# Performance work log

Hardware: AMD Instinct MI355X
Metric: run time of the kernel (lower is better)

The kernel has to match this reference:

```python
import jax, jax.numpy as jnp
import numpy as np

H, IN, L, R = 128, 64, 3, 7
Nc, Na, Nx = 10000, 40000, 100000
NS = (Nc, Na, Nx)
ES = (50000, 100000, 100000, 150000, 200000, 200000, 200000)
# relation order: cc, c->a, a->c, aa, a->x, x->a, xx  (0=core,1=agg,2=access)
SRC_T = (0, 0, 1, 1, 1, 2, 2)
DST_T = (0, 1, 0, 1, 2, 1, 2)


def setup_inputs() -> dict:
    key = jax.random.key(0)
    ks = iter(jax.random.split(key, 80))
    d = {}
    for name, n in (("x_core", Nc), ("x_agg", Na), ("x_access", Nx)):
        d[name] = jax.random.normal(next(ks), (n, IN), jnp.float32)
    for r in range(R):
        d[f"src{r}"] = jax.random.randint(next(ks), (ES[r],), 0, NS[SRC_T[r]])
        d[f"dst{r}"] = jax.random.randint(next(ks), (ES[r],), 0, NS[DST_T[r]])
        d[f"ea{r}"] = jax.random.normal(next(ks), (ES[r], 3), jnp.float32)

    def w(k, shape, fan):
        return (jax.random.normal(k, shape, jnp.float32) / np.float32(np.sqrt(fan)))

    for nt in ("core", "agg", "access"):
        d[f"linW_{nt}"] = w(next(ks), (IN, H), IN)
        d[f"linb_{nt}"] = jnp.zeros((H,), jnp.float32)
    d["eW"] = w(next(ks), (L, R, 3, H), 3)       # GINEConv edge Linear(3->H)
    d["eb"] = jnp.zeros((L, R, H), jnp.float32)
    d["W1"] = w(next(ks), (L, R, H, H), H)        # MLP first Linear
    d["b1"] = jnp.zeros((L, R, H), jnp.float32)
    d["g1"] = jnp.ones((L, R, H), jnp.float32)    # BatchNorm gamma
    d["be1"] = jnp.zeros((L, R, H), jnp.float32)  # BatchNorm beta
    d["W2"] = w(next(ks), (L, R, H, H), H)        # MLP second Linear
    d["b2"] = jnp.zeros((L, R, H), jnp.float32)
    return d


def _forward(x_core, x_agg, x_access,
             linW_core, linb_core, linW_agg, linb_agg, linW_access, linb_access,
             eW, eb, W1, b1, g1, be1, W2, b2, srcs, dsts, eas):
    elu = jax.nn.elu
    h = [elu(x_core @ linW_core + linb_core),
         elu(x_agg @ linW_agg + linb_agg),
         elu(x_access @ linW_access + linb_access)]
    bn_inv = 1.0 / jnp.sqrt(jnp.float32(1.0 + 1e-5))  # eval BN: running mean 0, var 1
    for l in range(L):
        out = [jnp.zeros_like(ht) for ht in h]
        for r in range(R):
            s, t = SRC_T[r], DST_T[r]
            # GINEConv message: ReLU(x_j + Lin(edge_attr))  -> [E, H]
            msg = jax.nn.relu(h[s][srcs[r]] + eas[r] @ eW[l, r] + eb[l, r])
            agg = jax.ops.segment_sum(msg, dsts[r], num_segments=h[t].shape[0])
            z = h[t] + agg  # (1+eps)*x_i + aggr, eps=0
            # PyG MLP([H,H,H]): Linear -> BatchNorm -> ReLU -> Linear
            z = jax.nn.relu((z @ W1[l, r] + b1[l, r]) * bn_inv * g1[l, r] + be1[l, r])
            out[t] = out[t] + (z @ W2[l, r] + b2[l, r])  # HeteroConv aggr='sum'
        # residual + ELU; dropout is identity in eval mode
        h = [elu(out[t] + h[t]) for t in range(3)]
    return tuple(h)


def reference(x_core, x_agg, x_access,
              src0, dst0, ea0, src1, dst1, ea1, src2, dst2, ea2,
              src3, dst3, ea3, src4, dst4, ea4, src5, dst5, ea5,
              src6, dst6, ea6,
              linW_core, linb_core, linW_agg, linb_agg, linW_access, linb_access,
              eW, eb, W1, b1, g1, be1, W2, b2):
    srcs = (src0, src1, src2, src3, src4, src5, src6)
    dsts = (dst0, dst1, dst2, dst3, dst4, dst5, dst6)
    eas = (ea0, ea1, ea2, ea3, ea4, ea5, ea6)
    return _forward(x_core, x_agg, x_access,
                    linW_core, linb_core, linW_agg, linb_agg, linW_access, linb_access,
                    eW, eb, W1, b1, g1, be1, W2, b2, srcs, dsts, eas)
```

## Files before the change

### kernel.cpp

```cpp
#include <hip/hip_runtime.h>
#include <math.h>

#define H 128

typedef __attribute__((ext_vector_type(8))) short short8;
typedef __attribute__((ext_vector_type(4))) float f32x4;

static const int SRC_T_[7] = {0, 0, 1, 1, 1, 2, 2};
static const int DST_T_[7] = {0, 1, 0, 1, 2, 1, 2};

__device__ __forceinline__ float eluf(float x) {
    return x > 0.f ? x : (__expf(x) - 1.f);
}
__device__ __forceinline__ unsigned short f2bf(float x) {
    union { float f; unsigned int u; } v; v.f = x;
    unsigned int r = v.u + 0x7fffu + ((v.u >> 16) & 1u);
    return (unsigned short)(r >> 16);
}
__device__ __forceinline__ float bf2f(unsigned int u) {
    union { unsigned int u; float f; } v; v.u = u << 16;
    return v.f;
}

#define GLDS16(gp, lp) __builtin_amdgcn_global_load_lds( \
    (const __attribute__((address_space(1))) void*)(gp), \
    (__attribute__((address_space(3))) void*)(lp), 16, 0, 0)

struct PreCtx {
    const int* dst[7];
    int* deg;
    int E[7], bOff[8], hOff[8];
    const float* W1; const float* W2; const float* linW[3];
    unsigned short* wp; unsigned short* wlin;
    int gEnd;
};

__global__ __launch_bounds__(256) void k_pre(PreCtx P)
{
    const int b = blockIdx.x;
    const int tid = threadIdx.x;

    if (b < P.hOff[7]) {
        int r = 0;
        while (b >= P.hOff[r + 1]) ++r;
        const int lb = b - P.hOff[r];
        const int nb = P.hOff[r + 1] - P.hOff[r];
        const int* dst = P.dst[r];
        int* degr = P.deg + (P.bOff[r] << 8);
        for (int e = lb * 256 + tid; e < P.E[r]; e += nb * 256)
            atomicAdd(&degr[dst[e]], 1);
        return;
    }
    {
        const int lb = b - P.hOff[7];
        const int gw = P.gEnd - P.hOff[7];
        for (int i = lb * 256 + tid; i < 21 * 16384; i += gw * 256) {
            int lr = i >> 14, rem = i & 16383;
            int c = rem >> 7, k = rem & 127;
            P.wp[(size_t)(lr * 2 + 0) * 16384 + rem] = f2bf(P.W1[(size_t)lr * 16384 + k * H + c]);
            P.wp[(size_t)(lr * 2 + 1) * 16384 + rem] = f2bf(P.W2[(size_t)lr * 16384 + k * H + c]);
        }
        for (int i = lb * 256 + tid; i < 3 * 8192; i += gw * 256) {
            int t = i >> 13, rem = i & 8191;
            int c = rem >> 6, k = rem & 63;
            P.wlin[t * 8192 + c * 64 + k] = f2bf(P.linW[t][k * H + c]);
        }
    }
}

struct InCtx {
    const float* x[3]; const float* linb[3];
    unsigned short* hb[3]; int n[3];
    int gend[3];
};

__global__ __launch_bounds__(512, 2) void k_input_mfma(
    InCtx I, const unsigned short* __restrict__ wlin)
{
    __shared__ unsigned short xb[128 * 64];
    __shared__ unsigned short ob[128 * H];

    const int b = blockIdx.x;
    const int t = (b >= I.gend[0] ? 1 : 0) + (b >= I.gend[1] ? 1 : 0);
    const int lb = b - (t == 0 ? 0 : I.gend[t - 1]);
    const int n = I.n[t];
    const int tid = threadIdx.x;
    const int lane = tid & 63;
    const int wave = tid >> 6;
    const int wr = wave >> 2;
    const int wc = wave & 3;
    const int l15 = lane & 15;
    const int lq  = lane >> 4;
    const int c0 = wc * 32 + l15;
    const int r0 = lb * 128;
    const int rows = min(128, n - r0);
    const float* x = I.x[t];

    for (int idx = tid; idx < 128 * 16; idx += 512) {
        const int row = idx >> 4, cg = (idx & 15) << 2;
        uint2 p;
        if (row < rows) {
            f32x4 v = *(const f32x4*)&x[(size_t)(r0 + row) * 64 + cg];
            p.x = (unsigned int)f2bf(v.x) | ((unsigned int)f2bf(v.y) << 16);
            p.y = (unsigned int)f2bf(v.z) | ((unsigned int)f2bf(v.w) << 16);
        } else { p.x = 0; p.y = 0; }
        *(uint2*)&xb[row * 64 + (cg ^ ((row & 7) << 3))] = p;
    }
    const unsigned short* wt = wlin + (size_t)t * 8192;
    short8 wf[2][2];
#pragma unroll
    for (int nf = 0; nf < 2; ++nf)
#pragma unroll
        for (int kc = 0; kc < 2; ++kc)
            wf[nf][kc] = *(const short8*)&wt[(c0 + nf * 16) * 64 + kc * 32 + (lq << 3)];
    const float bc0 = I.linb[t][c0], bc1 = I.linb[t][c0 + 16];
    __syncthreads();

    const f32x4 Z4 = {0.f, 0.f, 0.f, 0.f};
    f32x4 acc[4][2];
#pragma unroll
    for (int rb = 0; rb < 4; ++rb)
#pragma unroll
        for (int nf = 0; nf < 2; ++nf) acc[rb][nf] = Z4;
#pragma unroll
    for (int kc = 0; kc < 2; ++kc) {
        const int kb = kc * 32 + (lq << 3);
        short8 af[4];
#pragma unroll
        for (int rb = 0; rb < 4; ++rb) {
            const int row = wr * 64 + rb * 16 + l15;
            af[rb] = *(const short8*)&xb[row * 64 + (kb ^ ((row & 7) << 3))];
        }
#pragma unroll
        for (int rb = 0; rb < 4; ++rb)
#pragma unroll
            for (int nf = 0; nf < 2; ++nf)
                acc[rb][nf] = __builtin_amdgcn_mfma_f32_16x16x32_bf16(
                    af[rb], wf[nf][kc], acc[rb][nf], 0, 0, 0);
    }
#pragma unroll
    for (int rb = 0; rb < 4; ++rb)
#pragma unroll
        for (int nf = 0; nf < 2; ++nf) {
            const int col = c0 + nf * 16;
            const float bc = nf == 0 ? bc0 : bc1;
#pragma unroll
            for (int rg = 0; rg < 4; ++rg) {
                const int row = wr * 64 + rb * 16 + (lq << 2) + rg;
                ob[row * H + col] = f2bf(eluf(acc[rb][nf][rg] + bc));
            }
        }
    __syncthreads();
    uint2* d = (uint2*)&I.hb[t][(size_t)r0 * H];
    const uint2* s2 = (const uint2*)ob;
    for (int idx = tid; idx < rows * 32; idx += 512) d[idx] = s2[idx];
}

struct CsrCtx {
    const int* src[7]; const int* dst[7]; const float* ea[7];
    int* csr_src[7]; uint2* csr_ea[7]; int* ptr[7];
    int* deg; int* cursor; int* bsum;
    int eOff[8];
    int bOff[8];
    int nd[7];
};

__global__ __launch_bounds__(256) void k_scan_partial_all(CsrCtx C)
{
    __shared__ int s[256];
    const int b = blockIdx.x;
    int r = 0;
    while (b >= C.bOff[r + 1]) ++r;
    const int lb = b - C.bOff[r];
    const int tid = threadIdx.x;
    const int idx = lb * 256 + tid;
    s[tid] = idx < C.nd[r] ? C.deg[(C.bOff[r] << 8) + idx] : 0;
    __syncthreads();
    for (int off = 128; off > 0; off >>= 1) {
        if (tid < off) s[tid] += s[tid + off];
        __syncthreads();
    }
    if (tid == 0) C.bsum[b] = s[0];
}

__global__ __launch_bounds__(512) void k_scan_mid_all(CsrCtx C)
{
    __shared__ int s[512];
    const int r = blockIdx.x;
    const int nb = C.bOff[r + 1] - C.bOff[r];
    const int tid = threadIdx.x;
    const int v = tid < nb ? C.bsum[C.bOff[r] + tid] : 0;
    s[tid] = v;
    __syncthreads();
    for (int off = 1; off < 512; off <<= 1) {
        int t = (tid >= off) ? s[tid - off] : 0;
        __syncthreads();
        s[tid] += t;
        __syncthreads();
    }
    if (tid < nb) C.bsum[C.bOff[r] + tid] = s[tid] - v;
    if (tid == nb - 1) C.ptr[r][C.nd[r]] = s[tid];
}

__global__ __launch_bounds__(256) void k_scan_final_all(CsrCtx C)
{
    __shared__ int s[256];
    const int b = blockIdx.x;
    int r = 0;
    while (b >= C.bOff[r + 1]) ++r;
    const int lb = b - C.bOff[r];
    const int tid = threadIdx.x;
    const int idx = lb * 256 + tid;
    const int v = idx < C.nd[r] ? C.deg[(C.bOff[r] << 8) + idx] : 0;
    s[tid] = v;
    __syncthreads();
    for (int off = 1; off < 256; off <<= 1) {
        int t = (tid >= off) ? s[tid - off] : 0;
        __syncthreads();
        s[tid] += t;
        __syncthreads();
    }
    if (idx < C.nd[r]) {
        const int excl = s[tid] - v + C.bsum[b];
        C.ptr[r][idx] = excl;
        C.cursor[(C.bOff[r] << 8) + idx] = excl;
    }
}

__global__ __launch_bounds__(256) void k_scatter_all(CsrCtx C, int Etot)
{
    for (int e = blockIdx.x * 256 + threadIdx.x; e < Etot; e += gridDim.x * 256) {
        int r = 0;
        while (e >= C.eOff[r + 1]) ++r;
        const int le = e - C.eOff[r];
        const int d = C.dst[r][le];
        const int pos = atomicAdd(&C.cursor[(C.bOff[r] << 8) + d], 1);
        C.csr_src[r][pos] = C.src[r][le];
        const float* eap = C.ea[r] + (size_t)3 * le;
        uint2 p;
        p.x = (unsigned int)f2bf(eap[0]) | ((unsigned int)f2bf(eap[1]) << 16);
        p.y = (unsigned int)f2bf(eap[2]);
        C.csr_ea[r][pos] = p;
    }
}

struct AggCtx {
    const int* ptr[7]; const int* csr_src[7]; const uint2* csr_ea[7];
    const unsigned short* hsrc[7]; const unsigned short* hdst[7];
    unsigned short* z[7];
    int gOff[8];
    int nd[7];
};

__global__ __launch_bounds__(256) void k_aggz_all(
    AggCtx A, const float* __restrict__ eW, const float* __restrict__ eb, int l)
{
    const int b = blockIdx.x;
    int r = 0;
    while (b >= A.gOff[r + 1]) ++r;
    const int lb = b - A.gOff[r];
    const int wave = threadIdx.x >> 6;
    const int lane = threadIdx.x & 63;
    const int t2 = lane << 1;
    const int lr = l * 7 + r;
    const float* eWr = eW + (size_t)lr * 3 * H;
    const float* ebr = eb + (size_t)lr * H;
    const float w00 = eWr[t2],         w01 = eWr[t2 + 1];
    const float w10 = eWr[H + t2],     w11 = eWr[H + t2 + 1];
    const float w20 = eWr[2 * H + t2], w21 = eWr[2 * H + t2 + 1];
    const float b0 = ebr[t2], b1v = ebr[t2 + 1];

    const int nd = A.nd[r];
    const int d0 = lb * 64 + wave * 16;
    if (d0 >= nd) return;
    const int dend = min(d0 + 16, nd);
    const int* __restrict__ ptr = A.ptr[r];
    const int* __restrict__ cs = A.csr_src[r];
    const uint2* __restrict__ ce = A.csr_ea[r];
    const unsigned short* __restrict__ hs = A.hsrc[r];
    const unsigned short* __restrict__ hd = A.hdst[r];
    unsigned int* __restrict__ zp = (unsigned int*)A.z[r];

    int p1 = ptr[d0];
    for (int d = d0; d < dend; ++d) {
        const int p0v = p1;
        p1 = ptr[d + 1];
        const unsigned int hdv = ((const unsigned int*)&hd[(size_t)d * H])[lane];
        float acc0 = bf2f(hdv & 0xffffu);
        float acc1 = bf2f(hdv >> 16);
        int i = p0v;
        if (i + 1 < p1) {
            int s0 = cs[i], s1 = cs[i + 1];
            uint2 eC0 = ce[i], eC1 = ce[i + 1];
            unsigned int hvC0 = ((const unsigned int*)&hs[(size_t)s0 * H])[lane];
            unsigned int hvC1 = ((const unsigned int*)&hs[(size_t)s1 * H])[lane];
            for (;;) {
                const int jn = i + 2;
                const bool more = (jn + 1 < p1);
                uint2 eN0, eN1; unsigned int hvN0 = 0, hvN1 = 0;
                if (more) {
                    const int sN0 = cs[jn], sN1 = cs[jn + 1];
                    eN0 = ce[jn]; eN1 = ce[jn + 1];
                    hvN0 = ((const unsigned int*)&hs[(size_t)sN0 * H])[lane];
                    hvN1 = ((const unsigned int*)&hs[(size_t)sN1 * H])[lane];
                }
                const float a00 = bf2f(eC0.x & 0xffffu), a01 = bf2f(eC0.x >> 16), a02 = bf2f(eC0.y & 0xffffu);
                const float a10 = bf2f(eC1.x & 0xffffu), a11 = bf2f(eC1.x >> 16), a12 = bf2f(eC1.y & 0xffffu);
                acc0 += fmaxf(bf2f(hvC0 & 0xffffu) + a00 * w00 + a01 * w10 + a02 * w20 + b0, 0.f)
                      + fmaxf(bf2f(hvC1 & 0xffffu) + a10 * w00 + a11 * w10 + a12 * w20 + b0, 0.f);
                acc1 += fmaxf(bf2f(hvC0 >> 16) + a00 * w01 + a01 * w11 + a02 * w21 + b1v, 0.f)
                      + fmaxf(bf2f(hvC1 >> 16) + a10 * w01 + a11 * w11 + a12 * w21 + b1v, 0.f);
                i = jn;
                if (!more) break;
                eC0 = eN0; eC1 = eN1; hvC0 = hvN0; hvC1 = hvN1;
            }
        }
        if (i < p1) {
            const int s = cs[i];
            const uint2 ep = ce[i];
            const float a0 = bf2f(ep.x & 0xffffu);
            const float a1 = bf2f(ep.x >> 16);
            const float a2 = bf2f(ep.y & 0xffffu);
            const unsigned int hv = ((const unsigned int*)&hs[(size_t)s * H])[lane];
            acc0 += fmaxf(bf2f(hv & 0xffffu) + a0 * w00 + a1 * w10 + a2 * w20 + b0, 0.f);
            acc1 += fmaxf(bf2f(hv >> 16)     + a0 * w01 + a1 * w11 + a2 * w21 + b1v, 0.f);
        }
        zp[(size_t)d * 64 + (lane ^ ((d & 7) << 2))] =
            (unsigned int)f2bf(acc0) | ((unsigned int)f2bf(acc1) << 16);
    }
}

struct MlpCtx {
    const unsigned short* z[3][3];
    int lr[3][3];
    int nrel[3];
    int gend[3];
    int noffH[3];
    int n[3];
};

__global__ __launch_bounds__(512, 2) void k_mlp_all(
    MlpCtx M, const unsigned short* __restrict__ hb,
    unsigned short* __restrict__ hbw, float* __restrict__ fout,
    const unsigned short* __restrict__ wprep,
    const float* __restrict__ b1g, const float* __restrict__ g1g,
    const float* __restrict__ be1g, const float* __restrict__ b2g, int fin)
{
    __shared__ unsigned short smem[2 * 128 * H];
    unsigned short* zt  = smem;
    unsigned short* a1t = smem + 128 * H;

    const int b = blockIdx.x;
    const int t = (b >= M.gend[0] ? 1 : 0) + (b >= M.gend[1] ? 1 : 0);
    const int lb = b - (t == 0 ? 0 : M.gend[t - 1]);
    const int n = M.n[t];
    const int nrel = M.nrel[t];
    const unsigned short* hbp = hb + (size_t)M.noffH[t];

    const int tid = threadIdx.x;
    const int lane = tid & 63;
    const int wave = tid >> 6;
    const int wr = wave >> 2;
    const int wc = wave & 3;
    const int l15 = lane & 15;
    const int lq  = lane >> 4;
    const int c0 = wc * 32 + l15;

    const int r0 = lb * 128;
    const int rows = min(128, n - r0);
    const bool full = (rows == 128);

    auto stage = [&](const unsigned short* z) {
        const unsigned short* zsrc = z + (size_t)r0 * H;
        if (full) {
#pragma unroll
            for (int it = 0; it < 4; ++it) {
                const int off = (wave * 4 + it) * 512;
                GLDS16(zsrc + off + lane * 8, zt + off);
            }
        } else {
            for (int idx = tid; idx < rows * 16; idx += 512) {
                *(uint4*)&zt[idx * 8] = *(const uint4*)&zsrc[idx * 8];
            }
        }
    };

    const float bn_inv = 0.99999500003749977f;
    const f32x4 Z4 = {0.f, 0.f, 0.f, 0.f};
    f32x4 acc2[4][2];
#pragma unroll
    for (int rb = 0; rb < 4; ++rb)
#pragma unroll
        for (int nf = 0; nf < 2; ++nf) acc2[rb][nf] = Z4;
    float b2s0 = 0.f, b2s1 = 0.f;

    stage(M.z[t][0]);

    for (int rl = 0; rl < nrel; ++rl) {
        const int lr = M.lr[t][rl];
        const unsigned short* wp = wprep + (size_t)lr * 32768;
        short8 w1f[2][4], w2f[2][4];
#pragma unroll
        for (int nf = 0; nf < 2; ++nf)
#pragma unroll
            for (int kc = 0; kc < 4; ++kc) {
                w1f[nf][kc] = *(const short8*)&wp[(c0 + nf * 16) * H + kc * 32 + (lq << 3)];
                w2f[nf][kc] = *(const short8*)&wp[16384 + (c0 + nf * 16) * H + kc * 32 + (lq << 3)];
            }
        const float b1c0 = b1g[lr * H + c0],            b1c1 = b1g[lr * H + c0 + 16];
        const float sc0  = g1g[lr * H + c0] * bn_inv,   sc1  = g1g[lr * H + c0 + 16] * bn_inv;
        const float be0  = be1g[lr * H + c0],           be1v = be1g[lr * H + c0 + 16];
        b2s0 += b2g[lr * H + c0]; b2s1 += b2g[lr * H + c0 + 16];

        __syncthreads();

        f32x4 acc1[4][2];
#pragma unroll
        for (int rb = 0; rb < 4; ++rb)
#pragma unroll
            for (int nf = 0; nf < 2; ++nf) acc1[rb][nf] = Z4;
#pragma unroll
        for (int kc = 0; kc < 4; ++kc) {
            const int kb = kc * 32 + (lq << 3);
            short8 af[4];
#pragma unroll
            for (int rb = 0; rb < 4; ++rb) {
                const int row = wr * 64 + rb * 16 + l15;
                af[rb] = *(const short8*)&zt[row * H + (kb ^ ((row & 7) << 3))];
            }
#pragma unroll
            for (int rb = 0; rb < 4; ++rb)
#pragma unroll
                for (int nf = 0; nf < 2; ++nf)
                    acc1[rb][nf] = __builtin_amdgcn_mfma_f32_16x16x32_bf16(
                        af[rb], w1f[nf][kc], acc1[rb][nf], 0, 0, 0);
        }
#pragma unroll
        for (int rb = 0; rb < 4; ++rb)
#pragma unroll
            for (int nf = 0; nf < 2; ++nf) {
                const int col = c0 + nf * 16;
                const float b1c = nf == 0 ? b1c0 : b1c1;
                const float scv = nf == 0 ? sc0 : sc1;
                const float bev = nf == 0 ? be0 : be1v;
#pragma unroll
                for (int rg = 0; rg < 4; ++rg) {
                    const int row = wr * 64 + rb * 16 + (lq << 2) + rg;
                    float v = fmaxf((acc1[rb][nf][rg] + b1c) * scv + bev, 0.f);
                    a1t[row * H + (col ^ ((row & 7) << 3))] = f2bf(v);
                }
            }
        __syncthreads();

        if (rl + 1 < nrel) stage(M.z[t][rl + 1]);

#pragma unroll
        for (int kc = 0; kc < 4; ++kc) {
            const int kb = kc * 32 + (lq << 3);
            short8 af[4];
#pragma unroll
            for (int rb = 0; rb < 4; ++rb) {
                const int row = wr * 64 + rb * 16 + l15;
                af[rb] = *(const short8*)&a1t[row * H + (kb ^ ((row & 7) << 3))];
            }
#pragma unroll
            for (int rb = 0; rb < 4; ++rb)
#pragma unroll
                for (int nf = 0; nf < 2; ++nf)
                    acc2[rb][nf] = __builtin_amdgcn_mfma_f32_16x16x32_bf16(
                        af[rb], w2f[nf][kc], acc2[rb][nf], 0, 0, 0);
        }
    }

    if (fin) {
        float* fb = (float*)smem;
        float* foutp = fout + (size_t)M.noffH[t];
        __syncthreads();
#pragma unroll
        for (int rb = 0; rb < 4; ++rb)
#pragma unroll
            for (int nf = 0; nf < 2; ++nf) {
                const int col = c0 + nf * 16;
                const float b2s = nf == 0 ? b2s0 : b2s1;
#pragma unroll
                for (int rg = 0; rg < 4; ++rg) {
                    const int row = wr * 64 + rb * 16 + (lq << 2) + rg;
                    if (row < rows) {
                        const size_t o = (size_t)(r0 + row) * H + col;
                        fb[row * H + col] = eluf(acc2[rb][nf][rg] + b2s
                                                 + bf2f((unsigned int)hbp[o]));
                    }
                }
            }
        __syncthreads();
        float4* d4 = (float4*)&foutp[(size_t)r0 * H];
        const float4* s4 = (const float4*)fb;
        for (int idx = tid; idx < rows * 32; idx += 512) d4[idx] = s4[idx];
    } else {
        unsigned short* hbwp = hbw + (size_t)M.noffH[t];
        __syncthreads();
#pragma unroll
        for (int rb = 0; rb < 4; ++rb)
#pragma unroll
            for (int nf = 0; nf < 2; ++nf) {
                const int col = c0 + nf * 16;
                const float b2s = nf == 0 ? b2s0 : b2s1;
#pragma unroll
                for (int rg = 0; rg < 4; ++rg) {
                    const int row = wr * 64 + rb * 16 + (lq << 2) + rg;
                    if (row < rows) {
                        const size_t o = (size_t)(r0 + row) * H + col;
                        a1t[row * H + col] = f2bf(eluf(acc2[rb][nf][rg] + b2s
                                                       + bf2f((unsigned int)hbp[o])));
                    }
                }
            }
        __syncthreads();
        uint2* d = (uint2*)&hbwp[(size_t)r0 * H];
        const uint2* s2 = (const uint2*)a1t;
        for (int idx = tid; idx < rows * 32; idx += 512) d[idx] = s2[idx];
    }
}

static inline int imin(int a, int b) { return a < b ? a : b; }
static inline int imax(int a, int b) { return a > b ? a : b; }
static inline size_t alignup(size_t x) { return (x + 255) & ~(size_t)255; }

extern "C" void kernel_launch(void* const* d_in, const int* in_sizes, int n_in,
                              void* d_out, int out_size, void* d_ws, size_t ws_size,
                              hipStream_t stream) {
    const float* xin[3] = {(const float*)d_in[0], (const float*)d_in[1], (const float*)d_in[2]};
    const int* src[7]; const int* dst[7]; const float* ea[7]; int E[7];
    for (int r = 0; r < 7; ++r) {
        src[r] = (const int*)d_in[3 + 3 * r];
        dst[r] = (const int*)d_in[4 + 3 * r];
        ea[r]  = (const float*)d_in[5 + 3 * r];
        E[r]   = in_sizes[3 + 3 * r];
    }
    const float* linW[3] = {(const float*)d_in[24], (const float*)d_in[26], (const float*)d_in[28]};
    const float* linb[3] = {(const float*)d_in[25], (const float*)d_in[27], (const float*)d_in[29]};
    const float* eW  = (const float*)d_in[30];
    const float* ebp = (const float*)d_in[31];
    const float* W1  = (const float*)d_in[32];
    const float* b1  = (const float*)d_in[33];
    const float* g1  = (const float*)d_in[34];
    const float* be1 = (const float*)d_in[35];
    const float* W2  = (const float*)d_in[36];
    const float* b2  = (const float*)d_in[37];

    const int NSn[3]  = {in_sizes[0] / 64, in_sizes[1] / 64, in_sizes[2] / 64};
    const int NTOT = NSn[0] + NSn[1] + NSn[2];
    const int noff[3] = {0, NSn[0], NSn[0] + NSn[1]};

    float* fout = (float*)d_out;

    int eOff[8]; eOff[0] = 0;
    for (int r = 0; r < 7; ++r) eOff[r + 1] = eOff[r] + E[r];
    const int Etot = eOff[7];
    int bOff[8]; bOff[0] = 0;
    for (int r = 0; r < 7; ++r) bOff[r + 1] = bOff[r] + (NSn[DST_T_[r]] + 255) / 256;
    int gOff[8]; gOff[0] = 0;
    for (int r = 0; r < 7; ++r) gOff[r + 1] = gOff[r] + (NSn[DST_T_[r]] + 63) / 64;

    char* wsb = (char*)d_ws;
    size_t off = 0;
    unsigned short* hb = (unsigned short*)(wsb + off); off = alignup(off + (size_t)NTOT * H * 2);
    unsigned short* zb[7];
    for (int r = 0; r < 7; ++r) {
        int nd = NSn[DST_T_[r]];
        zb[r] = (unsigned short*)(wsb + off); off = alignup(off + (size_t)nd * H * 2);
    }
    unsigned short* wprep = (unsigned short*)(wsb + off); off = alignup(off + (size_t)21 * 32768 * 2);
    unsigned short* wlin  = (unsigned short*)(wsb + off); off = alignup(off + (size_t)3 * 8192 * 2);
    int* deg    = (int*)(wsb + off); off = alignup(off + (size_t)bOff[7] * 256 * 4);
    int* cursor = (int*)(wsb + off); off = alignup(off + (size_t)bOff[7] * 256 * 4);
    int* bsum   = (int*)(wsb + off); off = alignup(off + (size_t)bOff[7] * 4 + 256);
    int* ptrs[7]; int* csrs[7]; uint2* ceas[7];
    for (int r = 0; r < 7; ++r) {
        int nd = NSn[DST_T_[r]];
        ptrs[r] = (int*)(wsb + off); off = alignup(off + (size_t)(nd + 1) * 4);
    }
    for (int r = 0; r < 7; ++r) {
        csrs[r] = (int*)(wsb + off); off = alignup(off + (size_t)E[r] * 4);
    }
    for (int r = 0; r < 7; ++r) {
        ceas[r] = (uint2*)(wsb + off); off = alignup(off + (size_t)E[r] * 8);
    }

    PreCtx P;
    for (int r = 0; r < 7; ++r) { P.dst[r] = dst[r]; P.E[r] = E[r]; }
    P.deg = deg;
    for (int r = 0; r < 8; ++r) P.bOff[r] = bOff[r];
    P.hOff[0] = 0;
    for (int r = 0; r < 7; ++r)
        P.hOff[r + 1] = P.hOff[r] + imax(1, (E[r] + 1023) / 1024);
    P.W1 = W1; P.W2 = W2; P.wp = wprep; P.wlin = wlin;
    for (int t = 0; t < 3; ++t) P.linW[t] = linW[t];
    P.gEnd = P.hOff[7] + 256;

    hipMemsetAsync(deg, 0, (size_t)bOff[7] * 256 * 4, stream);
    k_pre<<<P.gEnd, 256, 0, stream>>>(P);

    InCtx I;
    int ig = 0;
    for (int t = 0; t < 3; ++t) {
        I.x[t] = xin[t]; I.linb[t] = linb[t];
        I.hb[t] = hb + (size_t)noff[t] * H; I.n[t] = NSn[t];
        ig += (NSn[t] + 127) / 128;
        I.gend[t] = ig;
    }
    k_input_mfma<<<ig, 512, 0, stream>>>(I, wlin);

    CsrCtx C;
    for (int r = 0; r < 7; ++r) {
        C.src[r] = src[r]; C.dst[r] = dst[r]; C.ea[r] = ea[r];
        C.csr_src[r] = csrs[r]; C.csr_ea[r] = ceas[r]; C.ptr[r] = ptrs[r];
        C.nd[r] = NSn[DST_T_[r]];
    }
    C.deg = deg; C.cursor = cursor; C.bsum = bsum;
    for (int r = 0; r < 8; ++r) { C.eOff[r] = eOff[r]; C.bOff[r] = bOff[r]; }

    k_scan_partial_all<<<bOff[7], 256, 0, stream>>>(C);
    k_scan_mid_all<<<7, 512, 0, stream>>>(C);
    k_scan_final_all<<<bOff[7], 256, 0, stream>>>(C);
    k_scatter_all<<<imin((Etot + 255) / 256, 8192), 256, 0, stream>>>(C, Etot);

    AggCtx A;
    for (int r = 0; r < 7; ++r) {
        A.ptr[r] = ptrs[r]; A.csr_src[r] = csrs[r]; A.csr_ea[r] = ceas[r];
        A.hsrc[r] = hb + (size_t)noff[SRC_T_[r]] * H;
        A.hdst[r] = hb + (size_t)noff[DST_T_[r]] * H;
        A.z[r] = zb[r];
        A.nd[r] = NSn[DST_T_[r]];
    }
    for (int r = 0; r < 8; ++r) A.gOff[r] = gOff[r];

    static const int RELS[3][3] = {{0, 2, 0}, {1, 3, 5}, {4, 6, 0}};
    static const int NRELS[3] = {2, 3, 2};
    MlpCtx M;
    int gend = 0;
    for (int t = 0; t < 3; ++t) {
        M.nrel[t] = NRELS[t];
        M.noffH[t] = noff[t] * H;
        M.n[t] = NSn[t];
        gend += (NSn[t] + 127) / 128;
        M.gend[t] = gend;
        for (int k = 0; k < 3; ++k) M.z[t][k] = zb[RELS[t][k]];
    }

    for (int l = 0; l < 3; ++l) {
        const int fin = (l == 2) ? 1 : 0;
        k_aggz_all<<<gOff[7], 256, 0, stream>>>(A, eW, ebp, l);
        for (int t = 0; t < 3; ++t)
            for (int k = 0; k < 3; ++k) M.lr[t][k] = l * 7 + RELS[t][k];
        k_mlp_all<<<M.gend[2], 512, 0, stream>>>(
            M, hb, hb, fout, wprep, b1, g1, be1, b2, fin);
    }
}
```

Measured before the change: 754.9 us.

## Pack CSR source index and edge attributes into one 16-byte record

Merges the separate CSR source-index and bf16 edge-attribute arrays into a single uint4 record per edge, so the aggregation kernel does one 16-byte load per edge instead of two dependent loads. The aggregation inner loop is changed from a 2-edge software-pipelined loop to a 4-edge batched loop that issues four record loads and four row gathers before computing. The scatter kernel now uses per-relation block ranges instead of a grid-stride loop with a per-edge relation search. In exchange, edge storage grows from 12 to 16 bytes and the scatter writes more bytes, and the cross-iteration prefetch is lost.

```diff
diff --git a/kernel.cpp b/kernel.cpp
--- a/kernel.cpp
+++ b/kernel.cpp
@@ -158,10 +158,11 @@
 
 struct CsrCtx {
     const int* src[7]; const int* dst[7]; const float* ea[7];
-    int* csr_src[7]; uint2* csr_ea[7]; int* ptr[7];
+    uint4* csr_rec[7]; int* ptr[7];
     int* deg; int* cursor; int* bsum;
-    int eOff[8];
+    int E[7];
     int bOff[8];
+    int sOff[8];
     int nd[7];
 };
 
@@ -227,25 +228,33 @@
     }
 }
 
-__global__ __launch_bounds__(256) void k_scatter_all(CsrCtx C, int Etot)
-{
-    for (int e = blockIdx.x * 256 + threadIdx.x; e < Etot; e += gridDim.x * 256) {
-        int r = 0;
-        while (e >= C.eOff[r + 1]) ++r;
-        const int le = e - C.eOff[r];
-        const int d = C.dst[r][le];
-        const int pos = atomicAdd(&C.cursor[(C.bOff[r] << 8) + d], 1);
-        C.csr_src[r][pos] = C.src[r][le];
-        const float* eap = C.ea[r] + (size_t)3 * le;
-        uint2 p;
-        p.x = (unsigned int)f2bf(eap[0]) | ((unsigned int)f2bf(eap[1]) << 16);
-        p.y = (unsigned int)f2bf(eap[2]);
-        C.csr_ea[r][pos] = p;
+__global__ __launch_bounds__(256) void k_scatter_all(CsrCtx C)
+{
+    const int b = blockIdx.x;
+    int r = 0;
+    while (b >= C.sOff[r + 1]) ++r;
+    const int lb = b - C.sOff[r];
+    const int nb = C.sOff[r + 1] - C.sOff[r];
+    const int* src = C.src[r];
+    const int* dst = C.dst[r];
+    const float* ea = C.ea[r];
+    int* cur = C.cursor + (C.bOff[r] << 8);
+    uint4* rec = C.csr_rec[r];
+    for (int e = lb * 256 + threadIdx.x; e < C.E[r]; e += nb * 256) {
+        const int d = dst[e];
+        const int pos = atomicAdd(&cur[d], 1);
+        const float* eap = ea + (size_t)3 * e;
+        uint4 p;
+        p.x = (unsigned int)src[e];
+        p.y = (unsigned int)f2bf(eap[0]) | ((unsigned int)f2bf(eap[1]) << 16);
+        p.z = (unsigned int)f2bf(eap[2]);
+        p.w = 0;
+        rec[pos] = p;
     }
 }
 
 struct AggCtx {
-    const int* ptr[7]; const int* csr_src[7]; const uint2* csr_ea[7];
+    const int* ptr[7]; const uint4* csr_rec[7];
     const unsigned short* hsrc[7]; const unsigned short* hdst[7];
     unsigned short* z[7];
     int gOff[8];
@@ -275,55 +284,48 @@
     if (d0 >= nd) return;
     const int dend = min(d0 + 16, nd);
     const int* __restrict__ ptr = A.ptr[r];
-    const int* __restrict__ cs = A.csr_src[r];
-    const uint2* __restrict__ ce = A.csr_ea[r];
+    const uint4* __restrict__ ce = A.csr_rec[r];
     const unsigned short* __restrict__ hs = A.hsrc[r];
     const unsigned short* __restrict__ hd = A.hdst[r];
     unsigned int* __restrict__ zp = (unsigned int*)A.z[r];
 
     int p1 = ptr[d0];
     for (int d = d0; d < dend; ++d) {
-        const int p0v = p1;
+        const int p0 = p1;
         p1 = ptr[d + 1];
         const unsigned int hdv = ((const unsigned int*)&hd[(size_t)d * H])[lane];
         float acc0 = bf2f(hdv & 0xffffu);
         float acc1 = bf2f(hdv >> 16);
-        int i = p0v;
-        if (i + 1 < p1) {
-            int s0 = cs[i], s1 = cs[i + 1];
-            uint2 eC0 = ce[i], eC1 = ce[i + 1];
-            unsigned int hvC0 = ((const unsigned int*)&hs[(size_t)s0 * H])[lane];
-            unsigned int hvC1 = ((const unsigned int*)&hs[(size_t)s1 * H])[lane];
-            for (;;) {
-                const int jn = i + 2;
-                const bool more = (jn + 1 < p1);
-                uint2 eN0, eN1; unsigned int hvN0 = 0, hvN1 = 0;
-                if (more) {
-                    const int sN0 = cs[jn], sN1 = cs[jn + 1];
-                    eN0 = ce[jn]; eN1 = ce[jn + 1];
-                    hvN0 = ((const unsigned int*)&hs[(size_t)sN0 * H])[lane];
-                    hvN1 = ((const unsigned int*)&hs[(size_t)sN1 * H])[lane];
-                }
-                const float a00 = bf2f(eC0.x & 0xffffu), a01 = bf2f(eC0.x >> 16), a02 = bf2f(eC0.y & 0xffffu);
-                const float a10 = bf2f(eC1.x & 0xffffu), a11 = bf2f(eC1.x >> 16), a12 = bf2f(eC1.y & 0xffffu);
-                acc0 += fmaxf(bf2f(hvC0 & 0xffffu) + a00 * w00 + a01 * w10 + a02 * w20 + b0, 0.f)
-                      + fmaxf(bf2f(hvC1 & 0xffffu) + a10 * w00 + a11 * w10 + a12 * w20 + b0, 0.f);
-                acc1 += fmaxf(bf2f(hvC0 >> 16) + a00 * w01 + a01 * w11 + a02 * w21 + b1v, 0.f)
-                      + fmaxf(bf2f(hvC1 >> 16) + a10 * w01 + a11 * w11 + a12 * w21 + b1v, 0.f);
-                i = jn;
-                if (!more) break;
-                eC0 = eN0; eC1 = eN1; hvC0 = hvN0; hvC1 = hvN1;
-            }
-        }
-        if (i < p1) {
-            const int s = cs[i];
-            const uint2 ep = ce[i];
-            const float a0 = bf2f(ep.x & 0xffffu);
-            const float a1 = bf2f(ep.x >> 16);
-            const float a2 = bf2f(ep.y & 0xffffu);
-            const unsigned int hv = ((const unsigned int*)&hs[(size_t)s * H])[lane];
-            acc0 += fmaxf(bf2f(hv & 0xffffu) + a0 * w00 + a1 * w10 + a2 * w20 + b0, 0.f);
-            acc1 += fmaxf(bf2f(hv >> 16)     + a0 * w01 + a1 * w11 + a2 * w21 + b1v, 0.f);
+        for (int i = p0; i < p1; i += 4) {
+            const int rem = p1 - i;
+            const int iB = rem > 1 ? i + 1 : i;
+            const int iC = rem > 2 ? i + 2 : i;
+            const int iD = rem > 3 ? i + 3 : i;
+            const uint4 rA = ce[i], rB = ce[iB], rC = ce[iC], rD = ce[iD];
+            const unsigned int hvA = ((const unsigned int*)&hs[(size_t)rA.x * H])[lane];
+            const unsigned int hvB = ((const unsigned int*)&hs[(size_t)rB.x * H])[lane];
+            const unsigned int hvC = ((const unsigned int*)&hs[(size_t)rC.x * H])[lane];
+            const unsigned int hvD = ((const unsigned int*)&hs[(size_t)rD.x * H])[lane];
+            {
+                const float a0 = bf2f(rA.y & 0xffffu), a1 = bf2f(rA.y >> 16), a2 = bf2f(rA.z & 0xffffu);
+                acc0 += fmaxf(bf2f(hvA & 0xffffu) + a0 * w00 + a1 * w10 + a2 * w20 + b0, 0.f);
+                acc1 += fmaxf(bf2f(hvA >> 16)     + a0 * w01 + a1 * w11 + a2 * w21 + b1v, 0.f);
+            }
+            if (rem > 1) {
+                const float a0 = bf2f(rB.y & 0xffffu), a1 = bf2f(rB.y >> 16), a2 = bf2f(rB.z & 0xffffu);
+                acc0 += fmaxf(bf2f(hvB & 0xffffu) + a0 * w00 + a1 * w10 + a2 * w20 + b0, 0.f);
+                acc1 += fmaxf(bf2f(hvB >> 16)     + a0 * w01 + a1 * w11 + a2 * w21 + b1v, 0.f);
+            }
+            if (rem > 2) {
+                const float a0 = bf2f(rC.y & 0xffffu), a1 = bf2f(rC.y >> 16), a2 = bf2f(rC.z & 0xffffu);
+                acc0 += fmaxf(bf2f(hvC & 0xffffu) + a0 * w00 + a1 * w10 + a2 * w20 + b0, 0.f);
+                acc1 += fmaxf(bf2f(hvC >> 16)     + a0 * w01 + a1 * w11 + a2 * w21 + b1v, 0.f);
+            }
+            if (rem > 3) {
+                const float a0 = bf2f(rD.y & 0xffffu), a1 = bf2f(rD.y >> 16), a2 = bf2f(rD.z & 0xffffu);
+                acc0 += fmaxf(bf2f(hvD & 0xffffu) + a0 * w00 + a1 * w10 + a2 * w20 + b0, 0.f);
+                acc1 += fmaxf(bf2f(hvD >> 16)     + a0 * w01 + a1 * w11 + a2 * w21 + b1v, 0.f);
+            }
         }
         zp[(size_t)d * 64 + (lane ^ ((d & 7) << 2))] =
             (unsigned int)f2bf(acc0) | ((unsigned int)f2bf(acc1) << 16);
@@ -554,9 +556,6 @@
 
     float* fout = (float*)d_out;
 
-    int eOff[8]; eOff[0] = 0;
-    for (int r = 0; r < 7; ++r) eOff[r + 1] = eOff[r] + E[r];
-    const int Etot = eOff[7];
     int bOff[8]; bOff[0] = 0;
     for (int r = 0; r < 7; ++r) bOff[r + 1] = bOff[r] + (NSn[DST_T_[r]] + 255) / 256;
     int gOff[8]; gOff[0] = 0;
@@ -575,16 +574,13 @@
     int* deg    = (int*)(wsb + off); off = alignup(off + (size_t)bOff[7] * 256 * 4);
     int* cursor = (int*)(wsb + off); off = alignup(off + (size_t)bOff[7] * 256 * 4);
     int* bsum   = (int*)(wsb + off); off = alignup(off + (size_t)bOff[7] * 4 + 256);
-    int* ptrs[7]; int* csrs[7]; uint2* ceas[7];
+    int* ptrs[7]; uint4* recs[7];
     for (int r = 0; r < 7; ++r) {
         int nd = NSn[DST_T_[r]];
         ptrs[r] = (int*)(wsb + off); off = alignup(off + (size_t)(nd + 1) * 4);
     }
     for (int r = 0; r < 7; ++r) {
-        csrs[r] = (int*)(wsb + off); off = alignup(off + (size_t)E[r] * 4);
-    }
-    for (int r = 0; r < 7; ++r) {
-        ceas[r] = (uint2*)(wsb + off); off = alignup(off + (size_t)E[r] * 8);
+        recs[r] = (uint4*)(wsb + off); off = alignup(off + (size_t)E[r] * 16);
     }
 
     PreCtx P;
@@ -614,20 +610,24 @@
     CsrCtx C;
     for (int r = 0; r < 7; ++r) {
         C.src[r] = src[r]; C.dst[r] = dst[r]; C.ea[r] = ea[r];
-        C.csr_src[r] = csrs[r]; C.csr_ea[r] = ceas[r]; C.ptr[r] = ptrs[r];
+        C.csr_rec[r] = recs[r]; C.ptr[r] = ptrs[r];
         C.nd[r] = NSn[DST_T_[r]];
+        C.E[r] = E[r];
     }
     C.deg = deg; C.cursor = cursor; C.bsum = bsum;
-    for (int r = 0; r < 8; ++r) { C.eOff[r] = eOff[r]; C.bOff[r] = bOff[r]; }
+    for (int r = 0; r < 8; ++r) C.bOff[r] = bOff[r];
+    C.sOff[0] = 0;
+    for (int r = 0; r < 7; ++r)
+        C.sOff[r + 1] = C.sOff[r] + imax(1, (E[r] + 1023) / 1024);
 
     k_scan_partial_all<<<bOff[7], 256, 0, stream>>>(C);
     k_scan_mid_all<<<7, 512, 0, stream>>>(C);
     k_scan_final_all<<<bOff[7], 256, 0, stream>>>(C);
-    k_scatter_all<<<imin((Etot + 255) / 256, 8192), 256, 0, stream>>>(C, Etot);
+    k_scatter_all<<<C.sOff[7], 256, 0, stream>>>(C);
 
     AggCtx A;
     for (int r = 0; r < 7; ++r) {
-        A.ptr[r] = ptrs[r]; A.csr_src[r] = csrs[r]; A.csr_ea[r] = ceas[r];
+        A.ptr[r] = ptrs[r]; A.csr_rec[r] = recs[r];
         A.hsrc[r] = hb + (size_t)noff[SRC_T_[r]] * H;
         A.hdst[r] = hb + (size_t)noff[DST_T_[r]] * H;
         A.z[r] = zb[r];
```

After: 783.6 us. +3.8%, slower.
